# Performance work log

Hardware: AMD Instinct MI355X
Metric: run time of the kernel (lower is better)

The kernel has to match this reference:

```python
import jax, jax.numpy as jnp
import numpy as np

B, S, H = 128, 512, 512

def _xavier(key, shape):
    fan_in, fan_out = shape[1], shape[0]
    limit = float(np.sqrt(6.0 / (fan_in + fan_out)))
    return jax.random.uniform(key, shape, jnp.float32, -limit, limit)

def setup_inputs() -> dict:
    key = jax.random.key(0)
    k1, k2, k3, k4, k5 = jax.random.split(key, 5)
    return {
        "h": jax.random.normal(k1, (B, S, H), jnp.float32),
        "x": jax.random.normal(k2, (B, S, H), jnp.float32),
        "Ve": _xavier(k3, (1, H)),
        "U1": _xavier(k4, (H, 2 * H)),
        "U2": _xavier(k5, (H, H)),
    }

def reference(h, x, Ve, U1, U2):
    # h: [B,S,H], x: [B,S,H]
    h_last = h[:, -1, :]                      # [B,H]
    U1a, U1b = U1[:, :U1.shape[0]], U1[:, U1.shape[0]:]  # each [H,H]
    # u1 = concat(h_t, h_last) @ U1.T, vectorized over t
    u1 = jnp.einsum('bsh,kh->bsk', h, U1a) + jnp.einsum('bh,kh->bk', h_last, U1b)[:, None, :]
    u2 = jnp.einsum('bsh,kh->bsk', x, U2)
    u = jnp.tanh(u1 + u2)                     # [B,S,H]
    e = jnp.einsum('bsk,k->bs', u, Ve[0])     # [B,S]
    alpha = jax.nn.softmax(e, axis=1)         # [B,S]
    context = jnp.einsum('bs,bsh->bh', alpha, h)
    return context
```

## Files before the change

kernel.cpp:

```cpp
#include <hip/hip_runtime.h>
#include <cstdint>
#include <cstddef>


typedef _Float16 h8 __attribute__((ext_vector_type(8)));
typedef float    f4 __attribute__((ext_vector_type(4)));

#define GLOAD16(g, l)                                                          \
  __builtin_amdgcn_global_load_lds(                                            \
      (const __attribute__((address_space(1))) void*)(g),                      \
      (__attribute__((address_space(3))) void*)(l), 16, 0, 0)

__global__ void bsetup_kernel(const float* __restrict__ U1, const float* __restrict__ U2,
                              _Float16* __restrict__ Bws) {
  int g = blockIdx.x * 256 + threadIdx.x;
  int s  = g & 7;
  int r  = (g >> 3) & 255;
  int kt = (g >> 11) & 15;
  int nt = g >> 15;
  int n = nt * 256 + r;
  int k = kt * 64 + ((s ^ (r & 7)) << 3);
  const float* p = (k < 512) ? (U1 + (size_t)n * 1024 + k)
                             : (U2 + (size_t)n * 512 + (k - 512));
  float4 a = *(const float4*)p;
  float4 b = *(const float4*)(p + 4);
  _Float16 hv[8];
  hv[0]=(_Float16)a.x; hv[1]=(_Float16)a.y; hv[2]=(_Float16)a.z; hv[3]=(_Float16)a.w;
  hv[4]=(_Float16)b.x; hv[5]=(_Float16)b.y; hv[6]=(_Float16)b.z; hv[7]=(_Float16)b.w;
  *(uint4*)(Bws + ((size_t)((nt * 16 + kt) * 256 + r) << 6) + (s << 3)) = *(uint4*)hv;
}

__global__ void bias_kernel(const float* __restrict__ hT, const float* __restrict__ U1,
                            float* __restrict__ bias) {
  const int b = blockIdx.x, t = threadIdx.x;
  const int l = t & 63, w = t >> 6;
  __shared__ float4 hl[128];
  if (t < 128) hl[t] = *(const float4*)(hT + ((size_t)b * 512 + 511) * 512 + t * 4);
  __syncthreads();
  for (int n = w; n < 512; n += 4) {
    const float4* ur = (const float4*)(U1 + (size_t)n * 1024 + 512);
    float4 u0 = ur[l],      u1 = ur[l + 64];
    float4 h0 = hl[l],      h1 = hl[l + 64];
    float s = u0.x*h0.x + u0.y*h0.y + u0.z*h0.z + u0.w*h0.w
            + u1.x*h1.x + u1.y*h1.y + u1.z*h1.z + u1.w*h1.w;
#pragma unroll
    for (int d = 1; d < 64; d <<= 1) s += __shfl_xor(s, d, 64);
    if (l == 0) bias[(size_t)b * 512 + n] = s;
  }
}

__global__ __launch_bounds__(256, 3)
void gemm_kernel(const float* __restrict__ hT, const float* __restrict__ xT,
                 const _Float16* __restrict__ Bws, const float* __restrict__ bias,
                 const float* __restrict__ Ve, float* __restrict__ e) {
  const int bid  = ((int)blockIdx.x & 7) * 256 + ((int)blockIdx.x >> 3);
  const int bm   = bid >> 1;
  const int nt   = bid & 1;
  const int row0 = bm * 64;
  const int bb   = row0 >> 9;
  const int t    = threadIdx.x;
  const int l    = t & 63;
  const int wv   = t >> 6;
  const int l15  = l & 15;
  const int lhi  = l >> 4;

  __shared__ __align__(16) float    Asm[64 * 64];
  __shared__ __align__(16) _Float16 Bsm[256 * 64];

  auto STAGE = [&](int kt) {
    const float* srcA = (kt < 8) ? hT : xT;
    const int kc = (kt & 7) * 64;
#pragma unroll
    for (int j = 0; j < 4; ++j) {
      int r = wv * 16 + j * 4 + (l >> 4);
      int s = l & 15;
      const float* g = srcA + (size_t)(row0 + r) * 512 + kc + ((s ^ (r & 7)) << 2);
      GLOAD16(g, &Asm[(wv * 16 + j * 4) * 64]);
    }
    const _Float16* tb = Bws + ((size_t)(nt * 16 + kt) << 14);
#pragma unroll
    for (int j = 0; j < 8; ++j) {
      const _Float16* g = tb + (wv * 8 + j) * 512 + l * 8;
      GLOAD16(g, &Bsm[(wv * 8 + j) * 512]);
    }
  };

  f4 acc[4][4];
#pragma unroll
  for (int mf = 0; mf < 4; ++mf)
#pragma unroll
    for (int nf = 0; nf < 4; ++nf)
      acc[mf][nf] = (f4){0.f, 0.f, 0.f, 0.f};

  STAGE(0);

  for (int kt = 0; kt < 16; ++kt) {
    __syncthreads();
#pragma unroll
    for (int kk = 0; kk < 2; ++kk) {
      h8 af[4], bf[4];
#pragma unroll
      for (int mf = 0; mf < 4; ++mf) {
        int rA = mf * 16 + l15;
        int c0 = kk * 8 + lhi * 2;
        const float4 a0 = *(const float4*)&Asm[rA * 64 + ((c0 ^ (rA & 7)) << 2)];
        const float4 a1 = *(const float4*)&Asm[rA * 64 + (((c0 + 1) ^ (rA & 7)) << 2)];
        h8 tf;
        tf[0]=(_Float16)a0.x; tf[1]=(_Float16)a0.y; tf[2]=(_Float16)a0.z; tf[3]=(_Float16)a0.w;
        tf[4]=(_Float16)a1.x; tf[5]=(_Float16)a1.y; tf[6]=(_Float16)a1.z; tf[7]=(_Float16)a1.w;
        af[mf] = tf;
      }
#pragma unroll
      for (int nf = 0; nf < 4; ++nf) {
        int rB = wv * 64 + nf * 16 + l15;
        int sB = kk * 4 + lhi;
        bf[nf] = *(const h8*)&Bsm[rB * 64 + ((sB ^ (rB & 7)) << 3)];
      }
#pragma unroll
      for (int mf = 0; mf < 4; ++mf)
#pragma unroll
        for (int nf = 0; nf < 4; ++nf)
          acc[mf][nf] = __builtin_amdgcn_mfma_f32_16x16x32_f16(af[mf], bf[nf], acc[mf][nf], 0, 0, 0);
    }
    __syncthreads();
    if (kt < 15) STAGE(kt + 1);
  }

  float vev[4], biasv[4];
#pragma unroll
  for (int nf = 0; nf < 4; ++nf) {
    int c = nt * 256 + wv * 64 + nf * 16 + l15;
    vev[nf]   = Ve[c];
    biasv[nf] = bias[(size_t)bb * 512 + c];
  }
#pragma unroll
  for (int mf = 0; mf < 4; ++mf) {
#pragma unroll
    for (int j = 0; j < 4; ++j) {
      float s = 0.f;
#pragma unroll
      for (int nf = 0; nf < 4; ++nf)
        s += tanhf(acc[mf][nf][j] + biasv[nf]) * vev[nf];
#pragma unroll
      for (int m = 1; m < 16; m <<= 1) s += __shfl_xor(s, m, 64);
      if (l15 == 0) atomicAdd(&e[row0 + mf * 16 + lhi * 4 + j], s);
    }
  }
}

__global__ void softmax_kernel(float* __restrict__ e) {
  const int b = blockIdx.x, t = threadIdx.x;
  float* row = e + (size_t)b * 512;
  float v0 = row[t], v1 = row[t + 256];
  float m = fmaxf(v0, v1);
#pragma unroll
  for (int d = 1; d < 64; d <<= 1) m = fmaxf(m, __shfl_xor(m, d, 64));
  __shared__ float r1[4], r2[4];
  if ((t & 63) == 0) r1[t >> 6] = m;
  __syncthreads();
  m = fmaxf(fmaxf(r1[0], r1[1]), fmaxf(r1[2], r1[3]));
  float e0 = expf(v0 - m), e1 = expf(v1 - m);
  float s = e0 + e1;
#pragma unroll
  for (int d = 1; d < 64; d <<= 1) s += __shfl_xor(s, d, 64);
  if ((t & 63) == 0) r2[t >> 6] = s;
  __syncthreads();
  s = r2[0] + r2[1] + r2[2] + r2[3];
  float inv = 1.0f / s;
  row[t]       = e0 * inv;
  row[t + 256] = e1 * inv;
}

__global__ __launch_bounds__(512)
void ctx_kernel(const float* __restrict__ hT, const float* __restrict__ alpha,
                float* __restrict__ out) {
  const int b  = blockIdx.x >> 2;
  const int sc = blockIdx.x & 3;
  const int hd = threadIdx.x;
  __shared__ float al[128];
  if (threadIdx.x < 128) al[threadIdx.x] = alpha[(size_t)b * 512 + sc * 128 + threadIdx.x];
  __syncthreads();
  const float* hp = hT + ((size_t)b * 512 + sc * 128) * 512 + hd;
  float acc = 0.f;
#pragma unroll 4
  for (int s = 0; s < 128; ++s) acc += al[s] * hp[(size_t)s * 512];
  atomicAdd(&out[b * 512 + hd], acc);
}

extern "C" void kernel_launch(void* const* d_in, const int* in_sizes, int n_in,
                              void* d_out, int out_size, void* d_ws, size_t ws_size,
                              hipStream_t stream) {
  const float* h  = (const float*)d_in[0];
  const float* x  = (const float*)d_in[1];
  const float* Ve = (const float*)d_in[2];
  const float* U1 = (const float*)d_in[3];
  const float* U2 = (const float*)d_in[4];
  float* out = (float*)d_out;

  _Float16* Bws  = (_Float16*)d_ws;
  float*    bias = (float*)((char*)d_ws + (1u << 20));
  float*    e    = (float*)((char*)d_ws + (1u << 20) + (256u << 10));
  if (ws_size < ((1u << 20) + (512u << 10))) return;

  hipMemsetAsync(e, 0, 65536 * sizeof(float), stream);
  hipMemsetAsync(d_out, 0, 65536 * sizeof(float), stream);

  bsetup_kernel<<<256, 256, 0, stream>>>(U1, U2, Bws);
  bias_kernel<<<128, 256, 0, stream>>>(h, U1, bias);
  gemm_kernel<<<2048, 256, 0, stream>>>(h, x, Bws, bias, Ve, e);
  softmax_kernel<<<128, 256, 0, stream>>>(e);
  ctx_kernel<<<512, 512, 0, stream>>>(h, e, out);
}
```

Baseline: 220.9 us.

## Retile GEMM to 128x128 with double-buffered fp16 LDS and register-staged A

The GEMM block tile changes from 64x256 to 128x128 with a 2x2 wave layout. A tiles are now loaded into registers, converted to fp16 once, and written into double-buffered LDS, while B tiles are prefetched asynchronously into the alternate buffer. Explicit vmcnt waits replace the two __syncthreads per k-step. The aim is to overlap global loads with MFMA work and to stop each wave from converting A from fp32 repeatedly. The cost is more registers and lower occupancy (launch bounds drop to 2 blocks per SIMD), and the hand-placed waitcnt counts must stay correct.

```diff
diff --git a/kernel.cpp b/kernel.cpp
--- a/kernel.cpp
+++ b/kernel.cpp
@@ -11,14 +11,20 @@
       (const __attribute__((address_space(1))) void*)(g),                      \
       (__attribute__((address_space(3))) void*)(l), 16, 0, 0)
 
+#define PIPE_BARRIER(N)                                                        \
+  do {                                                                         \
+    asm volatile("s_waitcnt vmcnt(" #N ") lgkmcnt(0)\n\ts_barrier" ::: "memory"); \
+    __builtin_amdgcn_sched_barrier(0);                                         \
+  } while (0)
+
 __global__ void bsetup_kernel(const float* __restrict__ U1, const float* __restrict__ U2,
                               _Float16* __restrict__ Bws) {
   int g = blockIdx.x * 256 + threadIdx.x;
   int s  = g & 7;
-  int r  = (g >> 3) & 255;
-  int kt = (g >> 11) & 15;
-  int nt = g >> 15;
-  int n = nt * 256 + r;
+  int r  = (g >> 3) & 127;
+  int kt = (g >> 10) & 15;
+  int nt = g >> 14;
+  int n = nt * 128 + r;
   int k = kt * 64 + ((s ^ (r & 7)) << 3);
   const float* p = (k < 512) ? (U1 + (size_t)n * 1024 + k)
                              : (U2 + (size_t)n * 512 + (k - 512));
@@ -27,7 +33,7 @@
   _Float16 hv[8];
   hv[0]=(_Float16)a.x; hv[1]=(_Float16)a.y; hv[2]=(_Float16)a.z; hv[3]=(_Float16)a.w;
   hv[4]=(_Float16)b.x; hv[5]=(_Float16)b.y; hv[6]=(_Float16)b.z; hv[7]=(_Float16)b.w;
-  *(uint4*)(Bws + ((size_t)((nt * 16 + kt) * 256 + r) << 6) + (s << 3)) = *(uint4*)hv;
+  *(uint4*)(Bws + ((size_t)g << 3)) = *(uint4*)hv;
 }
 
 __global__ void bias_kernel(const float* __restrict__ hT, const float* __restrict__ U1,
@@ -49,39 +55,49 @@
   }
 }
 
-__global__ __launch_bounds__(256, 3)
+__global__ __launch_bounds__(256, 2)
 void gemm_kernel(const float* __restrict__ hT, const float* __restrict__ xT,
                  const _Float16* __restrict__ Bws, const float* __restrict__ bias,
                  const float* __restrict__ Ve, float* __restrict__ e) {
   const int bid  = ((int)blockIdx.x & 7) * 256 + ((int)blockIdx.x >> 3);
-  const int bm   = bid >> 1;
-  const int nt   = bid & 1;
-  const int row0 = bm * 64;
+  const int bm   = bid >> 2;
+  const int nt   = bid & 3;
+  const int row0 = bm * 128;
   const int bb   = row0 >> 9;
   const int t    = threadIdx.x;
   const int l    = t & 63;
   const int wv   = t >> 6;
-  const int l15  = l & 15;
-  const int lhi  = l >> 4;
-
-  __shared__ __align__(16) float    Asm[64 * 64];
-  __shared__ __align__(16) _Float16 Bsm[256 * 64];
-
-  auto STAGE = [&](int kt) {
-    const float* srcA = (kt < 8) ? hT : xT;
-    const int kc = (kt & 7) * 64;
+  const int wm   = wv >> 1, wn = wv & 1;
+  const int l15  = l & 15, lhi = l >> 4;
+
+  __shared__ __align__(16) _Float16 Asm[2][8192];
+  __shared__ __align__(16) _Float16 Bsm[2][8192];
+
+  const int ar = t >> 1, ahf = t & 1;
+  const float* aRowH = hT + (size_t)(row0 + ar) * 512 + ahf * 32;
+  const float* aRowX = xT + (size_t)(row0 + ar) * 512 + ahf * 32;
+
+  f4 areg[2][8];
+
+  auto LOADA = [&](int buf, int k2) {
+    const float* p = ((k2 < 8) ? aRowH : aRowX) + (k2 & 7) * 64;
+#pragma unroll
+    for (int q = 0; q < 8; ++q) areg[buf][q] = *(const f4*)(p + q * 4);
+  };
+  auto GLOADB = [&](int c, int k2) {
+    const _Float16* tb = Bws + ((size_t)(nt * 16 + k2) << 13);
+#pragma unroll
+    for (int j = 0; j < 4; ++j)
+      GLOAD16(tb + j * 2048 + wv * 512 + (l << 3), &Bsm[c][j * 2048 + wv * 512]);
+  };
+  auto WRITEA = [&](int c, int buf) {
 #pragma unroll
     for (int j = 0; j < 4; ++j) {
-      int r = wv * 16 + j * 4 + (l >> 4);
-      int s = l & 15;
-      const float* g = srcA + (size_t)(row0 + r) * 512 + kc + ((s ^ (r & 7)) << 2);
-      GLOAD16(g, &Asm[(wv * 16 + j * 4) * 64]);
-    }
-    const _Float16* tb = Bws + ((size_t)(nt * 16 + kt) << 14);
-#pragma unroll
-    for (int j = 0; j < 8; ++j) {
-      const _Float16* g = tb + (wv * 8 + j) * 512 + l * 8;
-      GLOAD16(g, &Bsm[(wv * 8 + j) * 512]);
+      const f4 v0 = areg[buf][j * 2], v1 = areg[buf][j * 2 + 1];
+      _Float16 hv[8];
+      hv[0]=(_Float16)v0[0]; hv[1]=(_Float16)v0[1]; hv[2]=(_Float16)v0[2]; hv[3]=(_Float16)v0[3];
+      hv[4]=(_Float16)v1[0]; hv[5]=(_Float16)v1[1]; hv[6]=(_Float16)v1[2]; hv[7]=(_Float16)v1[3];
+      *(uint4*)&Asm[c][ar * 64 + ((((ahf << 2) + j) ^ (ar & 7)) << 3)] = *(uint4*)hv;
     }
   };
 
@@ -92,29 +108,29 @@
     for (int nf = 0; nf < 4; ++nf)
       acc[mf][nf] = (f4){0.f, 0.f, 0.f, 0.f};
 
-  STAGE(0);
-
+  LOADA(0, 0);
+  GLOADB(0, 0);
+  WRITEA(0, 0);
+  LOADA(1, 1);
+  PIPE_BARRIER(8);
+
+#pragma unroll
   for (int kt = 0; kt < 16; ++kt) {
-    __syncthreads();
+    const int c = kt & 1;
+    if (kt < 15) GLOADB(c ^ 1, kt + 1);
+    if (kt < 14) LOADA(c, kt + 2);
 #pragma unroll
     for (int kk = 0; kk < 2; ++kk) {
       h8 af[4], bf[4];
 #pragma unroll
       for (int mf = 0; mf < 4; ++mf) {
-        int rA = mf * 16 + l15;
-        int c0 = kk * 8 + lhi * 2;
-        const float4 a0 = *(const float4*)&Asm[rA * 64 + ((c0 ^ (rA & 7)) << 2)];
-        const float4 a1 = *(const float4*)&Asm[rA * 64 + (((c0 + 1) ^ (rA & 7)) << 2)];
-        h8 tf;
-        tf[0]=(_Float16)a0.x; tf[1]=(_Float16)a0.y; tf[2]=(_Float16)a0.z; tf[3]=(_Float16)a0.w;
-        tf[4]=(_Float16)a1.x; tf[5]=(_Float16)a1.y; tf[6]=(_Float16)a1.z; tf[7]=(_Float16)a1.w;
-        af[mf] = tf;
+        const int rA = wm * 64 + mf * 16 + l15;
+        af[mf] = *(const h8*)&Asm[c][rA * 64 + ((((kk << 2) + lhi) ^ (l15 & 7)) << 3)];
       }
 #pragma unroll
       for (int nf = 0; nf < 4; ++nf) {
-        int rB = wv * 64 + nf * 16 + l15;
-        int sB = kk * 4 + lhi;
-        bf[nf] = *(const h8*)&Bsm[rB * 64 + ((sB ^ (rB & 7)) << 3)];
+        const int rB = wn * 64 + nf * 16 + l15;
+        bf[nf] = *(const h8*)&Bsm[c][rB * 64 + ((((kk << 2) + lhi) ^ (l15 & 7)) << 3)];
       }
 #pragma unroll
       for (int mf = 0; mf < 4; ++mf)
@@ -122,16 +138,17 @@
         for (int nf = 0; nf < 4; ++nf)
           acc[mf][nf] = __builtin_amdgcn_mfma_f32_16x16x32_f16(af[mf], bf[nf], acc[mf][nf], 0, 0, 0);
     }
-    __syncthreads();
-    if (kt < 15) STAGE(kt + 1);
+    if (kt < 15) WRITEA(c ^ 1, c ^ 1);
+    if (kt < 14)       { PIPE_BARRIER(8); }
+    else if (kt == 14) { PIPE_BARRIER(0); }
   }
 
   float vev[4], biasv[4];
 #pragma unroll
   for (int nf = 0; nf < 4; ++nf) {
-    int c = nt * 256 + wv * 64 + nf * 16 + l15;
-    vev[nf]   = Ve[c];
-    biasv[nf] = bias[(size_t)bb * 512 + c];
+    int cidx = nt * 128 + wn * 64 + nf * 16 + l15;
+    vev[nf]   = Ve[cidx];
+    biasv[nf] = bias[(size_t)bb * 512 + cidx];
   }
 #pragma unroll
   for (int mf = 0; mf < 4; ++mf) {
@@ -143,7 +160,7 @@
         s += tanhf(acc[mf][nf][j] + biasv[nf]) * vev[nf];
 #pragma unroll
       for (int m = 1; m < 16; m <<= 1) s += __shfl_xor(s, m, 64);
-      if (l15 == 0) atomicAdd(&e[row0 + mf * 16 + lhi * 4 + j], s);
+      if (l15 == 0) atomicAdd(&e[row0 + wm * 64 + mf * 16 + lhi * 4 + j], s);
     }
   }
 }
```

Result: slower. 285.4 us (+29.2%).

## Pre-convert activations to fp16 and use a 128x128 GEMM tile

Applied to the files above, without the earlier changes.

When the workspace is large enough, h and x are first converted to fp16 buffers by a separate kernel. A new GEMM then stages fp16 A tiles directly into LDS with a 128x128 block tile and 2x2 wave layout, using a pre-arranged B image. The context reduction also reads the fp16 copy of h. The aim is to remove the per-tile fp32-to-fp16 conversion and the fp32 LDS footprint from the GEMM inner loop, at the cost of an extra full pass over the activations and reduced precision in the context sum.

```diff
diff --git a/kernel.cpp b/kernel.cpp
--- a/kernel.cpp
+++ b/kernel.cpp
@@ -11,8 +11,186 @@
       (const __attribute__((address_space(1))) void*)(g),                      \
       (__attribute__((address_space(3))) void*)(l), 16, 0, 0)
 
-__global__ void bsetup_kernel(const float* __restrict__ U1, const float* __restrict__ U2,
-                              _Float16* __restrict__ Bws) {
+__global__ __launch_bounds__(256)
+void cvt_kernel(const float* __restrict__ src, _Float16* __restrict__ dst, int n8) {
+  const int stride = gridDim.x * 256;
+  for (int i = blockIdx.x * 256 + threadIdx.x; i < n8; i += stride) {
+    const float* p = src + (size_t)i * 8;
+    f4 a = *(const f4*)p, b = *(const f4*)(p + 4);
+    _Float16 hv[8];
+    hv[0]=(_Float16)a[0]; hv[1]=(_Float16)a[1]; hv[2]=(_Float16)a[2]; hv[3]=(_Float16)a[3];
+    hv[4]=(_Float16)b[0]; hv[5]=(_Float16)b[1]; hv[6]=(_Float16)b[2]; hv[7]=(_Float16)b[3];
+    *(uint4*)(dst + (size_t)i * 8) = *(uint4*)hv;
+  }
+}
+
+__global__ void bsetup2_kernel(const float* __restrict__ U1, const float* __restrict__ U2,
+                               _Float16* __restrict__ Bimg) {
+  int g = blockIdx.x * 256 + threadIdx.x;
+  int l15 = g & 15;
+  int grp = (g >> 4) & 7;
+  int s   = (g >> 7) & 7;
+  int kt  = (g >> 10) & 15;
+  int nt  = g >> 14;
+  int n = nt * 128 + grp * 16 + l15;
+  int k = kt * 64 + s * 8;
+  const float* p = (k < 512) ? (U1 + (size_t)n * 1024 + k)
+                             : (U2 + (size_t)n * 512 + (k - 512));
+  f4 a = *(const f4*)p, b = *(const f4*)(p + 4);
+  _Float16 hv[8];
+  hv[0]=(_Float16)a[0]; hv[1]=(_Float16)a[1]; hv[2]=(_Float16)a[2]; hv[3]=(_Float16)a[3];
+  hv[4]=(_Float16)b[0]; hv[5]=(_Float16)b[1]; hv[6]=(_Float16)b[2]; hv[7]=(_Float16)b[3];
+  *(uint4*)(Bimg + (size_t)g * 8) = *(uint4*)hv;
+}
+
+__global__ void bias_kernel(const float* __restrict__ hT, const float* __restrict__ U1,
+                            float* __restrict__ bias) {
+  const int b = blockIdx.x, t = threadIdx.x;
+  const int l = t & 63, w = t >> 6;
+  __shared__ float4 hl[128];
+  if (t < 128) hl[t] = *(const float4*)(hT + ((size_t)b * 512 + 511) * 512 + t * 4);
+  __syncthreads();
+  for (int n = w; n < 512; n += 4) {
+    const float4* ur = (const float4*)(U1 + (size_t)n * 1024 + 512);
+    float4 u0 = ur[l],      u1 = ur[l + 64];
+    float4 h0 = hl[l],      h1 = hl[l + 64];
+    float s = u0.x*h0.x + u0.y*h0.y + u0.z*h0.z + u0.w*h0.w
+            + u1.x*h1.x + u1.y*h1.y + u1.z*h1.z + u1.w*h1.w;
+#pragma unroll
+    for (int d = 1; d < 64; d <<= 1) s += __shfl_xor(s, d, 64);
+    if (l == 0) bias[(size_t)b * 512 + n] = s;
+  }
+}
+
+__global__ __launch_bounds__(256, 3)
+void gemm2_kernel(const _Float16* __restrict__ hF, const _Float16* __restrict__ xF,
+                  const _Float16* __restrict__ Bimg, const float* __restrict__ bias,
+                  const float* __restrict__ Ve, float* __restrict__ e) {
+  const int bid  = ((int)blockIdx.x & 7) * 256 + ((int)blockIdx.x >> 3);
+  const int bm   = bid >> 2;
+  const int nt   = bid & 3;
+  const int row0 = bm * 128;
+  const int bb   = row0 >> 9;
+  const int t    = threadIdx.x;
+  const int l    = t & 63;
+  const int wv   = t >> 6;
+  const int wm   = wv >> 1, wn = wv & 1;
+  const int l15  = l & 15, lhi = l >> 4;
+
+  __shared__ __align__(16) _Float16 Asm[8192];
+  __shared__ __align__(16) _Float16 Bsm[8192];
+
+  const int aoff0 = (wv * 32 + (l >> 3)) * 512 + (((l & 7) ^ (l >> 3)) << 3);
+
+  auto STAGE = [&](int kt) {
+    const _Float16* ah = ((kt < 8) ? hF : xF) + (size_t)row0 * 512 + (kt & 7) * 64;
+#pragma unroll
+    for (int j = 0; j < 4; ++j)
+      GLOAD16(ah + aoff0 + j * 4096, &Asm[wv * 2048 + j * 512]);
+    const _Float16* bt = Bimg + ((size_t)(nt * 16 + kt) << 13);
+#pragma unroll
+    for (int j = 0; j < 4; ++j)
+      GLOAD16(bt + wv * 2048 + j * 512 + l * 8, &Bsm[wv * 2048 + j * 512]);
+  };
+
+  const int vA0 = wm * 4096 + l15 * 64 + (((0 + lhi) ^ (l15 & 7)) << 3);
+  const int vA1 = wm * 4096 + l15 * 64 + (((4 + lhi) ^ (l15 & 7)) << 3);
+  const int vB  = lhi * 1024 + wn * 512 + l15 * 8;
+
+  f4 acc[4][4];
+#pragma unroll
+  for (int mf = 0; mf < 4; ++mf)
+#pragma unroll
+    for (int nf = 0; nf < 4; ++nf)
+      acc[mf][nf] = (f4){0.f, 0.f, 0.f, 0.f};
+
+  STAGE(0);
+
+  for (int kt = 0; kt < 16; ++kt) {
+    __syncthreads();
+#pragma unroll
+    for (int kk = 0; kk < 2; ++kk) {
+      h8 af[4], bf[4];
+      const int a0 = (kk ? vA1 : vA0);
+#pragma unroll
+      for (int mf = 0; mf < 4; ++mf)
+        af[mf] = *(const h8*)&Asm[a0 + mf * 1024];
+#pragma unroll
+      for (int nf = 0; nf < 4; ++nf)
+        bf[nf] = *(const h8*)&Bsm[vB + kk * 4096 + nf * 128];
+#pragma unroll
+      for (int mf = 0; mf < 4; ++mf)
+#pragma unroll
+        for (int nf = 0; nf < 4; ++nf)
+          acc[mf][nf] = __builtin_amdgcn_mfma_f32_16x16x32_f16(af[mf], bf[nf], acc[mf][nf], 0, 0, 0);
+    }
+    __syncthreads();
+    if (kt < 15) STAGE(kt + 1);
+  }
+
+  float vev[4], biasv[4];
+#pragma unroll
+  for (int nf = 0; nf < 4; ++nf) {
+    int c = nt * 128 + wn * 64 + nf * 16 + l15;
+    vev[nf]   = Ve[c];
+    biasv[nf] = bias[(size_t)bb * 512 + c];
+  }
+#pragma unroll
+  for (int mf = 0; mf < 4; ++mf) {
+#pragma unroll
+    for (int j = 0; j < 4; ++j) {
+      float s = 0.f;
+#pragma unroll
+      for (int nf = 0; nf < 4; ++nf)
+        s += tanhf(acc[mf][nf][j] + biasv[nf]) * vev[nf];
+#pragma unroll
+      for (int m = 1; m < 16; m <<= 1) s += __shfl_xor(s, m, 64);
+      if (l15 == 0) atomicAdd(&e[row0 + wm * 64 + mf * 16 + lhi * 4 + j], s);
+    }
+  }
+}
+
+__global__ void softmax_kernel(float* __restrict__ e) {
+  const int b = blockIdx.x, t = threadIdx.x;
+  float* row = e + (size_t)b * 512;
+  float v0 = row[t], v1 = row[t + 256];
+  float m = fmaxf(v0, v1);
+#pragma unroll
+  for (int d = 1; d < 64; d <<= 1) m = fmaxf(m, __shfl_xor(m, d, 64));
+  __shared__ float r1[4], r2[4];
+  if ((t & 63) == 0) r1[t >> 6] = m;
+  __syncthreads();
+  m = fmaxf(fmaxf(r1[0], r1[1]), fmaxf(r1[2], r1[3]));
+  float e0 = expf(v0 - m), e1 = expf(v1 - m);
+  float s = e0 + e1;
+#pragma unroll
+  for (int d = 1; d < 64; d <<= 1) s += __shfl_xor(s, d, 64);
+  if ((t & 63) == 0) r2[t >> 6] = s;
+  __syncthreads();
+  s = r2[0] + r2[1] + r2[2] + r2[3];
+  float inv = 1.0f / s;
+  row[t]       = e0 * inv;
+  row[t + 256] = e1 * inv;
+}
+
+__global__ __launch_bounds__(512)
+void ctx16_kernel(const _Float16* __restrict__ hF, const float* __restrict__ alpha,
+                  float* __restrict__ out) {
+  const int b  = blockIdx.x >> 2;
+  const int sc = blockIdx.x & 3;
+  const int hd = threadIdx.x;
+  __shared__ float al[128];
+  if (threadIdx.x < 128) al[threadIdx.x] = alpha[(size_t)b * 512 + sc * 128 + threadIdx.x];
+  __syncthreads();
+  const _Float16* hp = hF + ((size_t)b * 512 + sc * 128) * 512 + hd;
+  float acc = 0.f;
+#pragma unroll 4
+  for (int s = 0; s < 128; ++s) acc += al[s] * (float)hp[(size_t)s * 512];
+  atomicAdd(&out[b * 512 + hd], acc);
+}
+
+__global__ void bsetup_fb(const float* __restrict__ U1, const float* __restrict__ U2,
+                          _Float16* __restrict__ Bws) {
   int g = blockIdx.x * 256 + threadIdx.x;
   int s  = g & 7;
   int r  = (g >> 3) & 255;
@@ -30,29 +208,10 @@
   *(uint4*)(Bws + ((size_t)((nt * 16 + kt) * 256 + r) << 6) + (s << 3)) = *(uint4*)hv;
 }
 
-__global__ void bias_kernel(const float* __restrict__ hT, const float* __restrict__ U1,
-                            float* __restrict__ bias) {
-  const int b = blockIdx.x, t = threadIdx.x;
-  const int l = t & 63, w = t >> 6;
-  __shared__ float4 hl[128];
-  if (t < 128) hl[t] = *(const float4*)(hT + ((size_t)b * 512 + 511) * 512 + t * 4);
-  __syncthreads();
-  for (int n = w; n < 512; n += 4) {
-    const float4* ur = (const float4*)(U1 + (size_t)n * 1024 + 512);
-    float4 u0 = ur[l],      u1 = ur[l + 64];
-    float4 h0 = hl[l],      h1 = hl[l + 64];
-    float s = u0.x*h0.x + u0.y*h0.y + u0.z*h0.z + u0.w*h0.w
-            + u1.x*h1.x + u1.y*h1.y + u1.z*h1.z + u1.w*h1.w;
-#pragma unroll
-    for (int d = 1; d < 64; d <<= 1) s += __shfl_xor(s, d, 64);
-    if (l == 0) bias[(size_t)b * 512 + n] = s;
-  }
-}
-
 __global__ __launch_bounds__(256, 3)
-void gemm_kernel(const float* __restrict__ hT, const float* __restrict__ xT,
-                 const _Float16* __restrict__ Bws, const float* __restrict__ bias,
-                 const float* __restrict__ Ve, float* __restrict__ e) {
+void gemm_fb(const float* __restrict__ hT, const float* __restrict__ xT,
+             const _Float16* __restrict__ Bws, const float* __restrict__ bias,
+             const float* __restrict__ Ve, float* __restrict__ e) {
   const int bid  = ((int)blockIdx.x & 7) * 256 + ((int)blockIdx.x >> 3);
   const int bm   = bid >> 1;
   const int nt   = bid & 1;
@@ -113,8 +272,7 @@
 #pragma unroll
       for (int nf = 0; nf < 4; ++nf) {
         int rB = wv * 64 + nf * 16 + l15;
-        int sB = kk * 4 + lhi;
-        bf[nf] = *(const h8*)&Bsm[rB * 64 + ((sB ^ (rB & 7)) << 3)];
+        bf[nf] = *(const h8*)&Bsm[rB * 64 + ((((kk << 2) + lhi) ^ (rB & 7)) << 3)];
       }
 #pragma unroll
       for (int mf = 0; mf < 4; ++mf)
@@ -148,32 +306,9 @@
   }
 }
 
-__global__ void softmax_kernel(float* __restrict__ e) {
-  const int b = blockIdx.x, t = threadIdx.x;
-  float* row = e + (size_t)b * 512;
-  float v0 = row[t], v1 = row[t + 256];
-  float m = fmaxf(v0, v1);
-#pragma unroll
-  for (int d = 1; d < 64; d <<= 1) m = fmaxf(m, __shfl_xor(m, d, 64));
-  __shared__ float r1[4], r2[4];
-  if ((t & 63) == 0) r1[t >> 6] = m;
-  __syncthreads();
-  m = fmaxf(fmaxf(r1[0], r1[1]), fmaxf(r1[2], r1[3]));
-  float e0 = expf(v0 - m), e1 = expf(v1 - m);
-  float s = e0 + e1;
-#pragma unroll
-  for (int d = 1; d < 64; d <<= 1) s += __shfl_xor(s, d, 64);
-  if ((t & 63) == 0) r2[t >> 6] = s;
-  __syncthreads();
-  s = r2[0] + r2[1] + r2[2] + r2[3];
-  float inv = 1.0f / s;
-  row[t]       = e0 * inv;
-  row[t + 256] = e1 * inv;
-}
-
 __global__ __launch_bounds__(512)
-void ctx_kernel(const float* __restrict__ hT, const float* __restrict__ alpha,
-                float* __restrict__ out) {
+void ctx_fb(const float* __restrict__ hT, const float* __restrict__ alpha,
+            float* __restrict__ out) {
   const int b  = blockIdx.x >> 2;
   const int sc = blockIdx.x & 3;
   const int hd = threadIdx.x;
@@ -197,17 +332,38 @@
   const float* U2 = (const float*)d_in[4];
   float* out = (float*)d_out;
 
-  _Float16* Bws  = (_Float16*)d_ws;
-  float*    bias = (float*)((char*)d_ws + (1u << 20));
-  float*    e    = (float*)((char*)d_ws + (1u << 20) + (256u << 10));
-  if (ws_size < ((1u << 20) + (512u << 10))) return;
-
-  hipMemsetAsync(e, 0, 65536 * sizeof(float), stream);
-  hipMemsetAsync(d_out, 0, 65536 * sizeof(float), stream);
-
-  bsetup_kernel<<<256, 256, 0, stream>>>(U1, U2, Bws);
-  bias_kernel<<<128, 256, 0, stream>>>(h, U1, bias);
-  gemm_kernel<<<2048, 256, 0, stream>>>(h, x, Bws, bias, Ve, e);
-  softmax_kernel<<<128, 256, 0, stream>>>(e);
-  ctx_kernel<<<512, 512, 0, stream>>>(h, e, out);
-}
+  const size_t MB = 1u << 20;
+
+  if (ws_size >= 130 * MB) {
+    _Float16* hF   = (_Float16*)d_ws;
+    _Float16* xF   = (_Float16*)((char*)d_ws + 64 * MB);
+    _Float16* Bimg = (_Float16*)((char*)d_ws + 128 * MB);
+    float*    bias = (float*)((char*)d_ws + 129 * MB);
+    float*    e    = (float*)((char*)d_ws + 129 * MB + 256 * 1024);
+
+    hipMemsetAsync(e, 0, 65536 * sizeof(float), stream);
+    hipMemsetAsync(d_out, 0, 65536 * sizeof(float), stream);
+
+    cvt_kernel<<<4096, 256, 0, stream>>>(h, hF, 4194304);
+    cvt_kernel<<<4096, 256, 0, stream>>>(x, xF, 4194304);
+    bsetup2_kernel<<<256, 256, 0, stream>>>(U1, U2, Bimg);
+    bias_kernel<<<128, 256, 0, stream>>>(h, U1, bias);
+    gemm2_kernel<<<2048, 256, 0, stream>>>(hF, xF, Bimg, bias, Ve, e);
+    softmax_kernel<<<128, 256, 0, stream>>>(e);
+    ctx16_kernel<<<512, 512, 0, stream>>>(hF, e, out);
+  } else {
+    if (ws_size < ((1u << 20) + (512u << 10))) return;
+    _Float16* Bws  = (_Float16*)d_ws;
+    float*    bias = (float*)((char*)d_ws + MB);
+    float*    e    = (float*)((char*)d_ws + MB + 256 * 1024);
+
+    hipMemsetAsync(e, 0, 65536 * sizeof(float), stream);
+    hipMemsetAsync(d_out, 0, 65536 * sizeof(float), stream);
+
+    bsetup_fb<<<256, 256, 0, stream>>>(U1, U2, Bws);
+    bias_kernel<<<128, 256, 0, stream>>>(h, U1, bias);
+    gemm_fb<<<2048, 256, 0, stream>>>(h, x, Bws, bias, Ve, e);
+    softmax_kernel<<<128, 256, 0, stream>>>(e);
+    ctx_fb<<<512, 512, 0, stream>>>(h, e, out);
+  }
+}
```

Result: slower. 269.1 us (+21.8%).
